# Performance work log

Measured on AMD Instinct MI355X. Metric: run time of the kernel, lower is better.

Reference implementation:

```python
import jax, jax.numpy as jnp
import numpy as np

B, C_IN, C_OUT, RANK, MODES, N = 32, 64, 64, 16, 64, 8192


def setup_inputs() -> dict:
    key = jax.random.key(0)
    k0, k1, k2, k3, k4 = jax.random.split(key, 5)
    x = jax.random.normal(k0, (B, C_IN, N), dtype=jnp.float32)
    U_r = jax.random.normal(k1, (C_IN, RANK), dtype=jnp.float32)
    U_i = jax.random.normal(k2, (C_IN, RANK), dtype=jnp.float32)
    V_r = jax.random.normal(k3, (RANK, C_OUT), dtype=jnp.float32)
    V_i = jax.random.normal(k4, (RANK, C_OUT), dtype=jnp.float32)
    S = jnp.ones((RANK,), dtype=jnp.float32)
    return {"x": x, "U_r": U_r, "U_i": U_i, "V_r": V_r, "V_i": V_i, "S": S}


def reference(x, U_r, U_i, V_r, V_i, S):
    # rFFT over spatial dim, orthonormal normalization (matches torch norm='ortho')
    x_fft = jnp.fft.rfft(x, axis=-1, norm='ortho')          # [B, C_in, N//2+1] complex
    n_freq = x_fft.shape[-1]
    modes = min(MODES, n_freq)
    x_modes = x_fft[..., :modes]                             # [B, C_in, modes]

    U = U_r + 1j * U_i                                       # [C_in, rank]
    V = V_r + 1j * V_i                                       # [rank, C_out]
    # w = (U * S) @ V, then slice first `modes` output channels (as in source)
    w = jnp.einsum('ir,ro->io', U * S[None, :].astype(U.dtype), V)
    w = w[..., :modes]                                       # no-op when C_out == modes

    out_modes = jnp.einsum('bix,io->box', x_modes, w)        # [B, C_out, modes]
    # zero-fill remaining spectrum (equivalent to zeros_like + slice assign)
    full = jnp.pad(out_modes, ((0, 0), (0, 0), (0, n_freq - modes)))
    return jnp.fft.irfft(full, n=x.shape[-1], axis=-1, norm='ortho')
```

## Files before the change

### kernel.cpp

```cpp
#include <hip/hip_runtime.h>

#define NPTS   8192
#define BATCH  32
#define CIN    64
#define COUT   64
#define RANKK  16
#define ROWS   (BATCH * CIN)
#define KB_SPLIT 16

typedef _Float16 f16;
typedef _Float16 f16x8 __attribute__((ext_vector_type(8)));
typedef float    f32x4 __attribute__((ext_vector_type(4)));

__device__ __forceinline__ void gload16(const void* g, void* l) {
  __builtin_amdgcn_global_load_lds(
      (const __attribute__((address_space(1))) void*)g,
      (__attribute__((address_space(3))) void*)l, 16, 0, 0);
}

__global__ __launch_bounds__(256) void build_tables(f16* __restrict__ T,
                                                    f16* __restrict__ Tt) {
  __shared__ f16 tile[128][18];
  const int n0 = blockIdx.x * 16;
  const int t = threadIdx.x;
#pragma unroll
  for (int j = 0; j < 8; ++j) {
    int flat = t + 256 * j;
    int c = flat >> 4, dn = flat & 15;
    int k = c & 63, n = n0 + dn;
    int m = (k * n) & (NPTS - 1);
    float ang = (float)m * (6.28318530717958647692f / (float)NPTS);
    float sv, cv;
    sincosf(ang, &sv, &cv);
    tile[c][dn] = (f16)((c < 64) ? cv : sv);
  }
  __syncthreads();
#pragma unroll
  for (int j = 0; j < 8; ++j) {
    int flat = t + 256 * j;
    int c = flat >> 4, dn = flat & 15;
    T[(size_t)c * NPTS + n0 + dn] = tile[c][dn];
  }
#pragma unroll
  for (int j = 0; j < 8; ++j) {
    int flat = t + 256 * j;
    int dn = flat >> 7, c = flat & 127;
    Tt[(size_t)(n0 + dn) * 128 + c] = tile[c][dn];
  }
}

__global__ __launch_bounds__(256) void fwd_dft(const float* __restrict__ x,
                                               const f16* __restrict__ T,
                                               float* __restrict__ Sp) {
  __shared__ __align__(16) char lds[3 * 16384];
  const int t    = threadIdx.x;
  const int w    = t >> 6;
  const int lane = t & 63;
  const int rl = lane & 15, hi = lane >> 4;
  const int kb = blockIdx.x & (KB_SPLIT - 1);
  const int r0 = (blockIdx.x >> 4) * 64;
  const int k0 = kb * (NPTS / KB_SPLIT);

  const int xc0 = t, xc1 = t + 256;
  const int tc0 = t, tc1 = t + 256;
  const int xr0_ = xc0 >> 3, xr1_ = xc1 >> 3;
  const int tr0_ = tc0 >> 2, tr1_ = tc1 >> 2;
  const int xo0 = ((xc0 & 7) ^ (xr0_ & 7)) << 2;
  const int xo1 = ((xc1 & 7) ^ (xr1_ & 7)) << 2;
  const int to0 = ((tc0 & 3) ^ (tr0_ & 3)) << 3;
  const int to1 = ((tc1 & 3) ^ (tr1_ & 3)) << 3;
  const float* xs0 = x + (size_t)(r0 + xr0_) * NPTS + k0 + xo0;
  const float* xs1 = x + (size_t)(r0 + xr1_) * NPTS + k0 + xo1;
  const f16*   ts0 = T + (size_t)tr0_ * NPTS + k0 + to0;
  const f16*   ts1 = T + (size_t)tr1_ * NPTS + k0 + to1;
  const int wu = w * 64 * 16;

  auto STAGE = [&](int kt, int slot) {
    char* xb = lds + slot * 16384;
    char* tb = xb + 8192;
    const int kk = kt * 32;
    gload16(xs0 + kk, xb + wu);
    gload16(xs1 + kk, xb + 4096 + wu);
    gload16(ts0 + kk, tb + wu);
    gload16(ts1 + kk, tb + 4096 + wu);
  };

  f32x4 acc[8];
#pragma unroll
  for (int i = 0; i < 8; ++i) acc[i] = (f32x4){0.f, 0.f, 0.f, 0.f};

  const int axr = w * 16 + rl;
  const int ad0 = (axr * 8 + ((2 * hi) ^ (axr & 7))) * 16;
  const int ad1 = (axr * 8 + ((2 * hi + 1) ^ (axr & 7))) * 16;
  int bd[8];
#pragma unroll
  for (int ct = 0; ct < 8; ++ct) {
    int trow = ct * 16 + rl;
    bd[ct] = (trow * 4 + (hi ^ (trow & 3))) * 16;
  }

  auto COMPUTE = [&](int slot) {
    char* xb = lds + slot * 16384;
    char* tb = xb + 8192;
    f32x4 a0 = *(const f32x4*)(xb + ad0);
    f32x4 a1 = *(const f32x4*)(xb + ad1);
    f16x8 af;
#pragma unroll
    for (int j = 0; j < 4; ++j) { af[j] = (f16)a0[j]; af[4 + j] = (f16)a1[j]; }
#pragma unroll
    for (int ct = 0; ct < 8; ++ct) {
      f16x8 bf = *(const f16x8*)(tb + bd[ct]);
      acc[ct] = __builtin_amdgcn_mfma_f32_16x16x32_f16(af, bf, acc[ct], 0, 0, 0);
    }
  };

  STAGE(0, 0);
  STAGE(1, 1);
  asm volatile("s_waitcnt vmcnt(4)" ::: "memory");
  __builtin_amdgcn_s_barrier();

  int sc = 0, ss = 2;
  for (int kt = 0; kt < 16; ++kt) {
    if (kt + 2 < 16) STAGE(kt + 2, ss);
    COMPUTE(sc);
    if (kt < 15) {
      if (kt + 2 < 16)
        asm volatile("s_waitcnt vmcnt(4)" ::: "memory");
      else
        asm volatile("s_waitcnt vmcnt(0)" ::: "memory");
      __builtin_amdgcn_s_barrier();
    }
    sc = (sc == 2) ? 0 : sc + 1;
    ss = (ss == 2) ? 0 : ss + 1;
  }

  float* out = Sp + ((size_t)kb * ROWS + r0 + w * 16) * 128;
#pragma unroll
  for (int ct = 0; ct < 8; ++ct)
#pragma unroll
    for (int i = 0; i < 4; ++i)
      out[(hi * 4 + i) * 128 + ct * 16 + rl] = acc[ct][i];
}

__global__ __launch_bounds__(256) void reduce_k(const float* __restrict__ Sp,
                                                float* __restrict__ Sred) {
  const int idx = blockIdx.x * 256 + threadIdx.x;
  const f32x4* src = (const f32x4*)Sp;
  f32x4 acc = src[idx];
#pragma unroll
  for (int s = 1; s < KB_SPLIT; ++s)
    acc += src[(size_t)s * (ROWS * 128 / 4) + idx];
  ((f32x4*)Sred)[idx] = acc;
}

__global__ __launch_bounds__(256) void mix3(const float* __restrict__ Sred,
                                            const float* __restrict__ Ur,
                                            const float* __restrict__ Ui,
                                            const float* __restrict__ Vr,
                                            const float* __restrict__ Vi,
                                            const float* __restrict__ Sv,
                                            f16* __restrict__ Qh) {
  __shared__ float Srs[64][64], Sis[64][64];
  __shared__ float wr_s[64][4], wi_s[64][4];
  const int b  = blockIdx.x >> 4;
  const int og = blockIdx.x & 15;
  const int t  = threadIdx.x;

#pragma unroll
  for (int j = 0; j < 8; ++j) {
    int f4 = t + 256 * j;
    int i = f4 >> 5, kc = (f4 & 31) * 4;
    f32x4 v = *(const f32x4*)(Sred + ((size_t)(b * 64 + i)) * 128 + kc);
    if (kc < 64) *(f32x4*)&Srs[i][kc] = v;
    else         *(f32x4*)&Sis[i][kc - 64] = v;
  }

  {
    int i = t >> 2, ol = t & 3, o = og * 4 + ol;
    float wr = 0.f, wi = 0.f;
#pragma unroll
    for (int r = 0; r < RANKK; ++r) {
      float ur = Ur[i * RANKK + r], ui = Ui[i * RANKK + r];
      float vr = Vr[r * COUT + o],  vi = Vi[r * COUT + o];
      float s = Sv[r];
      wr += s * (ur * vr - ui * vi);
      wi += s * (ur * vi + ui * vr);
    }
    wr_s[i][ol] = wr;
    wi_s[i][ol] = wi;
  }
  __syncthreads();

  const int ol = t >> 6, k = t & 63, o = og * 4 + ol;
  float qr = 0.f, qi = 0.f;
#pragma unroll 4
  for (int i = 0; i < 64; ++i) {
    float sr = Srs[i][k], si = Sis[i][k];
    float wr = wr_s[i][ol], wi = wi_s[i][ol];
    qr += sr * wr + si * wi;
    qi += sr * wi - si * wr;
  }
  float sk = (k == 0 ? 1.0f : 2.0f) / (float)NPTS;
  f16* qrow = Qh + ((size_t)(b * 64 + o)) * 128;
  qrow[k]      = (f16)(qr * sk);
  qrow[64 + k] = (f16)(-qi * sk);
}

__global__ __launch_bounds__(256) void inv_dft(const f16* __restrict__ Qh,
                                               const f16* __restrict__ Tt,
                                               float* __restrict__ y) {
  __shared__ f16   Bt[64][136];
  __shared__ float Tr[4][16][68];
  const int t = threadIdx.x, w = t >> 6, lane = t & 63;
  const int rl = lane & 15, hi = lane >> 4;
  const int nb = blockIdx.x & 127;
  const int rb = blockIdx.x >> 7;
  const int n0 = nb * 64, r0 = rb * 64;

  f16x8 stg[4];
#pragma unroll
  for (int j = 0; j < 4; ++j) {
    int d = j * 256 + t, row = d >> 4, q = d & 15;
    stg[j] = *(const f16x8*)(Tt + (size_t)(n0 + row) * 128 + q * 8);
  }
  const f16* qrow = Qh + (size_t)(r0 + w * 16 + rl) * 128 + 8 * hi;
  f16x8 af[4];
#pragma unroll
  for (int ksv = 0; ksv < 4; ++ksv) af[ksv] = *(const f16x8*)(qrow + ksv * 32);
#pragma unroll
  for (int j = 0; j < 4; ++j) {
    int d = j * 256 + t, row = d >> 4, q = d & 15;
    *(f16x8*)(&Bt[row][q * 8]) = stg[j];
  }
  __syncthreads();

  f32x4 acc[4];
#pragma unroll
  for (int i = 0; i < 4; ++i) acc[i] = (f32x4){0.f, 0.f, 0.f, 0.f};

#pragma unroll
  for (int ksv = 0; ksv < 4; ++ksv)
#pragma unroll
    for (int s = 0; s < 4; ++s) {
      f16x8 bf = *(const f16x8*)(&Bt[s * 16 + rl][(ksv * 4 + hi) * 8]);
      acc[s] = __builtin_amdgcn_mfma_f32_16x16x32_f16(af[ksv], bf, acc[s], 0, 0, 0);
    }

#pragma unroll
  for (int s = 0; s < 4; ++s)
#pragma unroll
    for (int i = 0; i < 4; ++i)
      Tr[w][hi * 4 + i][s * 16 + rl] = acc[s][i];
#pragma unroll
  for (int p = 0; p < 4; ++p) {
    int r = p * 4 + hi;
    f32x4 v = *(const f32x4*)(&Tr[w][r][rl * 4]);
    *(f32x4*)(y + (size_t)(r0 + w * 16 + r) * NPTS + n0 + rl * 4) = v;
  }
}

extern "C" void kernel_launch(void* const* d_in, const int* in_sizes, int n_in,
                              void* d_out, int out_size, void* d_ws, size_t ws_size,
                              hipStream_t stream) {
  const float* x  = (const float*)d_in[0];
  const float* Ur = (const float*)d_in[1];
  const float* Ui = (const float*)d_in[2];
  const float* Vr = (const float*)d_in[3];
  const float* Vi = (const float*)d_in[4];
  const float* Sv = (const float*)d_in[5];
  float* y = (float*)d_out;
  char* ws = (char*)d_ws;

  f16*   T    = (f16*)ws;
  f16*   Tt   = (f16*)(ws + (2u << 20));
  float* Sp   = (float*)(ws + (4u << 20));
  char*  p    = ws + (4u << 20) + (size_t)KB_SPLIT * ROWS * 128 * 4;
  float* Sred = (float*)p;
  f16*   Qh   = (f16*)(p + (size_t)ROWS * 128 * 4);

  build_tables<<<NPTS / 16, 256, 0, stream>>>(T, Tt);
  fwd_dft<<<(ROWS / 64) * KB_SPLIT, 256, 0, stream>>>(x, T, Sp);
  reduce_k<<<ROWS * 128 / 4 / 256, 256, 0, stream>>>(Sp, Sred);
  mix3<<<BATCH * 16, 256, 0, stream>>>(Sred, Ur, Ui, Vr, Vi, Sv, Qh);
  inv_dft<<<(ROWS / 64) * (NPTS / 64), 256, 0, stream>>>(Qh, Tt, y);
}
```

Baseline: 52.06 us.

## Retile forward DFT to 32-row blocks and inverse DFT to 128-row blocks

The forward DFT kernel now handles 32 rows per block instead of 64, with four waves split two by two over row halves and column groups. This doubles the grid to 1024 blocks and shrinks LDS per stage, trading more reloads of the twiddle table for more parallelism. The inverse DFT now processes 128 rows per block, so each staged twiddle tile is reused by two row tiles per wave. That halves the twiddle table reads and the number of blocks, at the cost of more registers per thread.

```diff
diff --git a/kernel.cpp b/kernel.cpp
--- a/kernel.cpp
+++ b/kernel.cpp
@@ -52,71 +52,69 @@
 __global__ __launch_bounds__(256) void fwd_dft(const float* __restrict__ x,
                                                const f16* __restrict__ T,
                                                float* __restrict__ Sp) {
-  __shared__ __align__(16) char lds[3 * 16384];
+  __shared__ __align__(16) char lds[3 * 12288];
   const int t    = threadIdx.x;
   const int w    = t >> 6;
   const int lane = t & 63;
   const int rl = lane & 15, hi = lane >> 4;
   const int kb = blockIdx.x & (KB_SPLIT - 1);
-  const int r0 = (blockIdx.x >> 4) * 64;
+  const int r0 = (blockIdx.x >> 4) * 32;
   const int k0 = kb * (NPTS / KB_SPLIT);
-
-  const int xc0 = t, xc1 = t + 256;
-  const int tc0 = t, tc1 = t + 256;
-  const int xr0_ = xc0 >> 3, xr1_ = xc1 >> 3;
-  const int tr0_ = tc0 >> 2, tr1_ = tc1 >> 2;
-  const int xo0 = ((xc0 & 7) ^ (xr0_ & 7)) << 2;
-  const int xo1 = ((xc1 & 7) ^ (xr1_ & 7)) << 2;
-  const int to0 = ((tc0 & 3) ^ (tr0_ & 3)) << 3;
+  const int h  = w & 1;
+  const int cg = w >> 1;
+
+  const int xr_ = t >> 3;
+  const int xo_ = ((t & 7) ^ (xr_ & 7)) << 2;
+  const int tc1 = t + 256;
+  const int tr0_ = t >> 2, tr1_ = tc1 >> 2;
+  const int to0 = ((t & 3) ^ (tr0_ & 3)) << 3;
   const int to1 = ((tc1 & 3) ^ (tr1_ & 3)) << 3;
-  const float* xs0 = x + (size_t)(r0 + xr0_) * NPTS + k0 + xo0;
-  const float* xs1 = x + (size_t)(r0 + xr1_) * NPTS + k0 + xo1;
+  const float* xs0 = x + (size_t)(r0 + xr_) * NPTS + k0 + xo_;
   const f16*   ts0 = T + (size_t)tr0_ * NPTS + k0 + to0;
   const f16*   ts1 = T + (size_t)tr1_ * NPTS + k0 + to1;
-  const int wu = w * 64 * 16;
+  const int wu = w * 1024;
 
   auto STAGE = [&](int kt, int slot) {
-    char* xb = lds + slot * 16384;
-    char* tb = xb + 8192;
+    char* xb = lds + slot * 12288;
+    char* tb = xb + 4096;
     const int kk = kt * 32;
     gload16(xs0 + kk, xb + wu);
-    gload16(xs1 + kk, xb + 4096 + wu);
     gload16(ts0 + kk, tb + wu);
     gload16(ts1 + kk, tb + 4096 + wu);
   };
 
-  f32x4 acc[8];
-#pragma unroll
-  for (int i = 0; i < 8; ++i) acc[i] = (f32x4){0.f, 0.f, 0.f, 0.f};
-
-  const int axr = w * 16 + rl;
+  f32x4 acc[4];
+#pragma unroll
+  for (int i = 0; i < 4; ++i) acc[i] = (f32x4){0.f, 0.f, 0.f, 0.f};
+
+  const int axr = h * 16 + rl;
   const int ad0 = (axr * 8 + ((2 * hi) ^ (axr & 7))) * 16;
   const int ad1 = (axr * 8 + ((2 * hi + 1) ^ (axr & 7))) * 16;
-  int bd[8];
-#pragma unroll
-  for (int ct = 0; ct < 8; ++ct) {
-    int trow = ct * 16 + rl;
-    bd[ct] = (trow * 4 + (hi ^ (trow & 3))) * 16;
+  int bd[4];
+#pragma unroll
+  for (int s = 0; s < 4; ++s) {
+    int trow = (cg * 4 + s) * 16 + rl;
+    bd[s] = (trow * 4 + (hi ^ (trow & 3))) * 16;
   }
 
   auto COMPUTE = [&](int slot) {
-    char* xb = lds + slot * 16384;
-    char* tb = xb + 8192;
+    char* xb = lds + slot * 12288;
+    char* tb = xb + 4096;
     f32x4 a0 = *(const f32x4*)(xb + ad0);
     f32x4 a1 = *(const f32x4*)(xb + ad1);
     f16x8 af;
 #pragma unroll
     for (int j = 0; j < 4; ++j) { af[j] = (f16)a0[j]; af[4 + j] = (f16)a1[j]; }
 #pragma unroll
-    for (int ct = 0; ct < 8; ++ct) {
-      f16x8 bf = *(const f16x8*)(tb + bd[ct]);
-      acc[ct] = __builtin_amdgcn_mfma_f32_16x16x32_f16(af, bf, acc[ct], 0, 0, 0);
+    for (int s = 0; s < 4; ++s) {
+      f16x8 bf = *(const f16x8*)(tb + bd[s]);
+      acc[s] = __builtin_amdgcn_mfma_f32_16x16x32_f16(af, bf, acc[s], 0, 0, 0);
     }
   };
 
   STAGE(0, 0);
   STAGE(1, 1);
-  asm volatile("s_waitcnt vmcnt(4)" ::: "memory");
+  asm volatile("s_waitcnt vmcnt(3)" ::: "memory");
   __builtin_amdgcn_s_barrier();
 
   int sc = 0, ss = 2;
@@ -125,7 +123,7 @@
     COMPUTE(sc);
     if (kt < 15) {
       if (kt + 2 < 16)
-        asm volatile("s_waitcnt vmcnt(4)" ::: "memory");
+        asm volatile("s_waitcnt vmcnt(3)" ::: "memory");
       else
         asm volatile("s_waitcnt vmcnt(0)" ::: "memory");
       __builtin_amdgcn_s_barrier();
@@ -134,12 +132,12 @@
     ss = (ss == 2) ? 0 : ss + 1;
   }
 
-  float* out = Sp + ((size_t)kb * ROWS + r0 + w * 16) * 128;
-#pragma unroll
-  for (int ct = 0; ct < 8; ++ct)
+  float* out = Sp + ((size_t)kb * ROWS + r0 + h * 16) * 128 + cg * 64;
+#pragma unroll
+  for (int s = 0; s < 4; ++s)
 #pragma unroll
     for (int i = 0; i < 4; ++i)
-      out[(hi * 4 + i) * 128 + ct * 16 + rl] = acc[ct][i];
+      out[(hi * 4 + i) * 128 + s * 16 + rl] = acc[s][i];
 }
 
 __global__ __launch_bounds__(256) void reduce_k(const float* __restrict__ Sp,
@@ -215,7 +213,7 @@
   const int rl = lane & 15, hi = lane >> 4;
   const int nb = blockIdx.x & 127;
   const int rb = blockIdx.x >> 7;
-  const int n0 = nb * 64, r0 = rb * 64;
+  const int n0 = nb * 64, r0 = rb * 128;
 
   f16x8 stg[4];
 #pragma unroll
@@ -223,10 +221,14 @@
     int d = j * 256 + t, row = d >> 4, q = d & 15;
     stg[j] = *(const f16x8*)(Tt + (size_t)(n0 + row) * 128 + q * 8);
   }
-  const f16* qrow = Qh + (size_t)(r0 + w * 16 + rl) * 128 + 8 * hi;
-  f16x8 af[4];
-#pragma unroll
-  for (int ksv = 0; ksv < 4; ++ksv) af[ksv] = *(const f16x8*)(qrow + ksv * 32);
+  f16x8 af[2][4];
+#pragma unroll
+  for (int rt2 = 0; rt2 < 2; ++rt2) {
+    const f16* qrow = Qh + (size_t)(r0 + w * 32 + rt2 * 16 + rl) * 128 + 8 * hi;
+#pragma unroll
+    for (int ksv = 0; ksv < 4; ++ksv)
+      af[rt2][ksv] = *(const f16x8*)(qrow + ksv * 32);
+  }
 #pragma unroll
   for (int j = 0; j < 4; ++j) {
     int d = j * 256 + t, row = d >> 4, q = d & 15;
@@ -234,28 +236,34 @@
   }
   __syncthreads();
 
-  f32x4 acc[4];
-#pragma unroll
-  for (int i = 0; i < 4; ++i) acc[i] = (f32x4){0.f, 0.f, 0.f, 0.f};
+  f32x4 acc[2][4];
+#pragma unroll
+  for (int r2 = 0; r2 < 2; ++r2)
+#pragma unroll
+    for (int i = 0; i < 4; ++i) acc[r2][i] = (f32x4){0.f, 0.f, 0.f, 0.f};
 
 #pragma unroll
   for (int ksv = 0; ksv < 4; ++ksv)
 #pragma unroll
     for (int s = 0; s < 4; ++s) {
       f16x8 bf = *(const f16x8*)(&Bt[s * 16 + rl][(ksv * 4 + hi) * 8]);
-      acc[s] = __builtin_amdgcn_mfma_f32_16x16x32_f16(af[ksv], bf, acc[s], 0, 0, 0);
-    }
-
-#pragma unroll
-  for (int s = 0; s < 4; ++s)
-#pragma unroll
-    for (int i = 0; i < 4; ++i)
-      Tr[w][hi * 4 + i][s * 16 + rl] = acc[s][i];
-#pragma unroll
-  for (int p = 0; p < 4; ++p) {
-    int r = p * 4 + hi;
-    f32x4 v = *(const f32x4*)(&Tr[w][r][rl * 4]);
-    *(f32x4*)(y + (size_t)(r0 + w * 16 + r) * NPTS + n0 + rl * 4) = v;
+      acc[0][s] = __builtin_amdgcn_mfma_f32_16x16x32_f16(af[0][ksv], bf, acc[0][s], 0, 0, 0);
+      acc[1][s] = __builtin_amdgcn_mfma_f32_16x16x32_f16(af[1][ksv], bf, acc[1][s], 0, 0, 0);
+    }
+
+#pragma unroll
+  for (int rt2 = 0; rt2 < 2; ++rt2) {
+#pragma unroll
+    for (int s = 0; s < 4; ++s)
+#pragma unroll
+      for (int i = 0; i < 4; ++i)
+        Tr[w][hi * 4 + i][s * 16 + rl] = acc[rt2][s][i];
+#pragma unroll
+    for (int p = 0; p < 4; ++p) {
+      int r = p * 4 + hi;
+      f32x4 v = *(const f32x4*)(&Tr[w][r][rl * 4]);
+      *(f32x4*)(y + (size_t)(r0 + w * 32 + rt2 * 16 + r) * NPTS + n0 + rl * 4) = v;
+    }
   }
 }
 
@@ -279,8 +287,8 @@
   f16*   Qh   = (f16*)(p + (size_t)ROWS * 128 * 4);
 
   build_tables<<<NPTS / 16, 256, 0, stream>>>(T, Tt);
-  fwd_dft<<<(ROWS / 64) * KB_SPLIT, 256, 0, stream>>>(x, T, Sp);
+  fwd_dft<<<(ROWS / 32) * KB_SPLIT, 256, 0, stream>>>(x, T, Sp);
   reduce_k<<<ROWS * 128 / 4 / 256, 256, 0, stream>>>(Sp, Sred);
   mix3<<<BATCH * 16, 256, 0, stream>>>(Sred, Ur, Ui, Vr, Vi, Sv, Qh);
-  inv_dft<<<(ROWS / 64) * (NPTS / 64), 256, 0, stream>>>(Qh, Tt, y);
-}
+  inv_dft<<<(ROWS / 128) * (NPTS / 64), 256, 0, stream>>>(Qh, Tt, y);
+}
```

After: 54.00 us. +3.7%, slower.
